# Kernel optimization log

Measured on AMD Instinct MI355X. Metric: run time of the kernel, lower is better.

The kernel has to match this reference:

```python
import jax, jax.numpy as jnp
import numpy as np

WINDOW_SIZE = 11
DATA_RANGE = 1.0
CHANNELS = 3


def _gaussian_window(window_size=WINDOW_SIZE, channel=CHANNELS):
    # 1D gaussian with sigma=1.0, normalized, then outer product -> 2D window
    x = np.arange(window_size)
    g = np.exp(-(x - window_size // 2) ** 2 / (2.0 * 1.0 ** 2))
    g = g / g.sum()
    w2d = np.outer(g, g)  # [K, K]
    # depthwise kernel in OIHW: [C, 1, K, K]
    w = np.broadcast_to(w2d, (channel, 1, window_size, window_size)).copy()
    return jnp.asarray(w, dtype=jnp.float32)


def _depthwise_conv(x, window):
    pad = WINDOW_SIZE // 2
    return jax.lax.conv_general_dilated(
        x, window,
        window_strides=(1, 1),
        padding=[(pad, pad), (pad, pad)],
        feature_group_count=CHANNELS,
        dimension_numbers=("NCHW", "OIHW", "NCHW"),
    )


def setup_inputs() -> dict:
    key = jax.random.key(0)
    k1, k2 = jax.random.split(key)
    pred = jax.random.uniform(k1, (16, 3, 512, 512), dtype=jnp.float32)
    target = jax.random.uniform(k2, (16, 3, 512, 512), dtype=jnp.float32)
    return {"pred": pred, "target": target}


def reference(pred, target):
    window = _gaussian_window()
    mu_x = _depthwise_conv(pred, window)
    mu_y = _depthwise_conv(target, window)
    sigma_x = _depthwise_conv(pred * pred, window) - mu_x * mu_x
    sigma_y = _depthwise_conv(target * target, window) - mu_y * mu_y
    sigma_xy = _depthwise_conv(pred * target, window) - mu_x * mu_y
    C1 = (0.01 * DATA_RANGE) ** 2
    C2 = (0.03 * DATA_RANGE) ** 2
    # NOTE: faithful to source, which (non-standardly) squares the variances in the denominator
    ssim_map = (2 * mu_x * mu_y + C1) * (2 * sigma_xy + C2) / (
        (mu_x * mu_x + mu_y * mu_y + C1) * (sigma_x * sigma_x + sigma_y * sigma_y + C2)
    )
    return ssim_map.mean()
```

## Files before the change

kernel.cpp:

```cpp
#include <hip/hip_runtime.h>
#include <stdint.h>


#define HH 512
#define WW 512
#define PLANES 48
#define TW 64
#define TH 16
#define RR 5
#define KK 11
#define HALO_W 74
#define TRP 28
#define RBW 76
#define NBLOCKS (PLANES * (WW / TW) * (HH / TH))
#define NTHREADS 256
#define NSTAGE (HALO_W * 7)
#define NITEMS1 (HALO_W * 2)
#define TOTAL_ELEMS (PLANES * HH * WW)

typedef _Float16 half2v __attribute__((ext_vector_type(2)));
typedef float float2v __attribute__((ext_vector_type(2)));

constexpr float G_[KK] = {
    1.4867195147342977e-06f, 1.3383022576488537e-04f, 4.4318484119380075e-03f,
    5.3990966513188063e-02f, 2.4197072451914337e-01f, 3.9894228040143270e-01f,
    2.4197072451914337e-01f, 5.3990966513188063e-02f, 4.4318484119380075e-03f,
    1.3383022576488537e-04f, 1.4867195147342977e-06f};

__device__ __forceinline__ half2v u2h(uint32_t u) {
  return __builtin_bit_cast(half2v, u);
}
__device__ __forceinline__ uint32_t packrtn(float a, float b) {
  half2v h = {(_Float16)a, (_Float16)b};
  return __builtin_bit_cast(uint32_t, h);
}

__global__ __launch_bounds__(NTHREADS, 4) void ssim_tile_kernel(
    const float* __restrict__ pred, const float* __restrict__ targ,
    float* __restrict__ partial) {
  __shared__ __align__(16) float spT[HALO_W][TRP];
  __shared__ __align__(16) float stT[HALO_W][TRP];
  __shared__ __align__(16) uint2 rbAB[TH][RBW];
  __shared__ __align__(16) float rbC[TH][RBW];
  __shared__ float wsums[4];

  const int tid = threadIdx.x;
  const int bid = blockIdx.x;
  const int plane = bid >> 8;
  const int tile = bid & 255;
  const int x0 = (tile & 7) * TW;
  const int y0 = (tile >> 3) * TH;
  const float* pp = pred + (size_t)plane * (HH * WW);
  const float* tp = targ + (size_t)plane * (HH * WW);

  const bool interior = (x0 >= 64) && (x0 <= 384) && (y0 >= 16) && (y0 <= 480);

  if (interior) {
    for (int i = tid; i < NSTAGE; i += NTHREADS) {
      const int c = i % HALO_W;
      const int rg = i / HALO_W;
      const float* pb = pp + (y0 - RR + 4 * rg) * WW + (x0 - RR + c);
      const float* tb = tp + (y0 - RR + 4 * rg) * WW + (x0 - RR + c);
      float4 pv, tv;
      pv.x = pb[0]; pv.y = pb[WW]; pv.z = pb[2 * WW]; pv.w = pb[3 * WW];
      tv.x = tb[0]; tv.y = tb[WW]; tv.z = tb[2 * WW]; tv.w = tb[3 * WW];
      *reinterpret_cast<float4*>(&spT[c][4 * rg]) = pv;
      *reinterpret_cast<float4*>(&stT[c][4 * rg]) = tv;
    }
  } else {
    for (int i = tid; i < NSTAGE; i += NTHREADS) {
      const int c = i % HALO_W;
      const int rg = i / HALO_W;
      const int gx = x0 - RR + c;
      const bool xok = (gx >= 0) && (gx < WW);
      float4 pv = make_float4(0.f, 0.f, 0.f, 0.f);
      float4 tv = pv;
      if (xok) {
#pragma unroll
        for (int w = 0; w < 4; ++w) {
          const int gy = y0 - RR + 4 * rg + w;
          if (gy >= 0 && gy < HH) {
            reinterpret_cast<float*>(&pv)[w] = pp[gy * WW + gx];
            reinterpret_cast<float*>(&tv)[w] = tp[gy * WW + gx];
          }
        }
      }
      *reinterpret_cast<float4*>(&spT[c][4 * rg]) = pv;
      *reinterpret_cast<float4*>(&stT[c][4 * rg]) = tv;
    }
  }
  __syncthreads();

  if (tid < NITEMS1) {
    const int c = (tid < HALO_W) ? tid : (tid - HALO_W);
    const int g = (tid < HALO_W) ? 0 : 1;
    const int yb = g * 8;

    float pv[20], tv[20];
#pragma unroll
    for (int h = 0; h < 5; ++h) {
      *reinterpret_cast<float4*>(&pv[4 * h]) =
          *reinterpret_cast<const float4*>(&spT[c][yb + 4 * h]);
      *reinterpret_cast<float4*>(&tv[4 * h]) =
          *reinterpret_cast<const float4*>(&stT[c][yb + 4 * h]);
    }

    float2v s01[8] = {{0,0},{0,0},{0,0},{0,0},{0,0},{0,0},{0,0},{0,0}};
    float2v s23[8] = {{0,0},{0,0},{0,0},{0,0},{0,0},{0,0},{0,0},{0,0}};
    float s4[8] = {0,0,0,0,0,0,0,0};
#pragma unroll
    for (int q = 0; q < 18; ++q) {
      const float a = pv[q];
      const float b = tv[q];
      const float2v av = {a, b};
      const float2v sq = av * av;
      const float ab = a * b;
#pragma unroll
      for (int j = 0; j < 8; ++j) {
        if (q < j || q > j + 10) continue;
        const float w = G_[q - j];
        const float2v w2 = {w, w};
        s01[j] = __builtin_elementwise_fma(w2, av, s01[j]);
        s23[j] = __builtin_elementwise_fma(w2, sq, s23[j]);
        s4[j] = fmaf(w, ab, s4[j]);
      }
    }

#pragma unroll
    for (int j = 0; j < 8; ++j) {
      uint2 u;
      u.x = packrtn(s01[j].x, s01[j].y);
      u.y = packrtn(s23[j].x, s23[j].y);
      rbAB[yb + j][c] = u;
      rbC[yb + j][c] = s4[j];
    }
  }
  __syncthreads();

  float lsum = 0.f;
  {
    const int m = tid & 15;
    const int y = tid >> 4;
    const int cb = m << 2;

    uint2 qv[14];
#pragma unroll
    for (int h = 0; h < 7; ++h) {
      uint4 w = *reinterpret_cast<const uint4*>(&rbAB[y][cb + 2 * h]);
      qv[2*h]   = make_uint2(w.x, w.y);
      qv[2*h+1] = make_uint2(w.z, w.w);
    }
    float cv[16];
#pragma unroll
    for (int h = 0; h < 4; ++h) {
      *reinterpret_cast<float4*>(&cv[4*h]) =
          *reinterpret_cast<const float4*>(&rbC[y][cb + 4 * h]);
    }

    float2v fa[14], fb[14];
#pragma unroll
    for (int k = 0; k < 14; ++k) {
      half2v ha = u2h(qv[k].x), hb = u2h(qv[k].y);
      fa[k] = float2v{(float)ha.x, (float)ha.y};
      fb[k] = float2v{(float)hb.x, (float)hb.y};
    }

    float2v accA[4], accB[4];
    float sC[4];
#pragma unroll
    for (int j = 0; j < 4; ++j) {
      float2v a = {0, 0}, b = {0, 0};
      float c = 0.f;
#pragma unroll
      for (int k = 0; k < KK; ++k) {
        const float2v w2 = {G_[k], G_[k]};
        a = __builtin_elementwise_fma(w2, fa[j + k], a);
        b = __builtin_elementwise_fma(w2, fb[j + k], b);
        c = fmaf(G_[k], cv[j + k], c);
      }
      accA[j] = a; accB[j] = b; sC[j] = c;
    }

    const float C1 = 1.0e-4f;
    const float C2 = 9.0e-4f;
#pragma unroll
    for (int j = 0; j < 4; ++j) {
      const float mu_x = accA[j].x;
      const float mu_y = accA[j].y;
      const float2v sv = __builtin_elementwise_fma(-accA[j], accA[j], accB[j]);
      const float sxy = sC[j] - mu_x * mu_y;
      const float num = (2.f * mu_x * mu_y + C1) * (2.f * sxy + C2);
      const float den = (mu_x * mu_x + mu_y * mu_y + C1) *
                        (fmaf(sv.x, sv.x, fmaf(sv.y, sv.y, C2)));
      lsum = fmaf(num, __builtin_amdgcn_rcpf(den), lsum);
    }
  }

#pragma unroll
  for (int off = 32; off > 0; off >>= 1) lsum += __shfl_xor(lsum, off, 64);
  if ((tid & 63) == 0) wsums[tid >> 6] = lsum;
  __syncthreads();
  if (tid == 0)
    partial[bid] = (wsums[0] + wsums[1]) + (wsums[2] + wsums[3]);
}

__global__ __launch_bounds__(1024) void ssim_reduce_kernel(
    const float* __restrict__ partial, float* __restrict__ out) {
  float s = 0.f;
  for (int i = threadIdx.x; i < NBLOCKS; i += 1024) s += partial[i];
#pragma unroll
  for (int off = 32; off > 0; off >>= 1) s += __shfl_xor(s, off, 64);
  __shared__ float ws[16];
  if ((threadIdx.x & 63) == 0) ws[threadIdx.x >> 6] = s;
  __syncthreads();
  if (threadIdx.x == 0) {
    float t = 0.f;
#pragma unroll
    for (int i = 0; i < 16; ++i) t += ws[i];
    out[0] = t * (1.0f / (float)TOTAL_ELEMS);
  }
}

extern "C" void kernel_launch(void* const* d_in, const int* in_sizes, int n_in,
                              void* d_out, int out_size, void* d_ws,
                              size_t ws_size, hipStream_t stream) {
  const float* pred = (const float*)d_in[0];
  const float* targ = (const float*)d_in[1];
  float* out = (float*)d_out;
  float* partial = (float*)d_ws;

  ssim_tile_kernel<<<NBLOCKS, NTHREADS, 0, stream>>>(pred, targ, partial);
  ssim_reduce_kernel<<<1, 1024, 0, stream>>>(partial, out);
}
```

Measured before the change: 67.19 us.

## Store vertical-pass intermediates in fp32 instead of packed fp16 and restructure staging loop

The intermediate row buffers for mu and second moments are now kept as fp32 float2 arrays instead of packed half precision, which removes the pack and unpack conversions and the fp16 rounding error on the intermediate sums. The staging loop replaces its div/mod indexing with incremental column and row-group stepping. In exchange, shared memory per block grows, which may lower occupancy, and the second pass issues more LDS reads.

```diff
diff --git a/kernel.cpp b/kernel.cpp
--- a/kernel.cpp
+++ b/kernel.cpp
@@ -11,14 +11,13 @@
 #define KK 11
 #define HALO_W 74
 #define TRP 28
-#define RBW 76
+#define RBW 74
+#define RCW 76
 #define NBLOCKS (PLANES * (WW / TW) * (HH / TH))
 #define NTHREADS 256
-#define NSTAGE (HALO_W * 7)
 #define NITEMS1 (HALO_W * 2)
 #define TOTAL_ELEMS (PLANES * HH * WW)
 
-typedef _Float16 half2v __attribute__((ext_vector_type(2)));
 typedef float float2v __attribute__((ext_vector_type(2)));
 
 constexpr float G_[KK] = {
@@ -27,21 +26,14 @@
     2.4197072451914337e-01f, 5.3990966513188063e-02f, 4.4318484119380075e-03f,
     1.3383022576488537e-04f, 1.4867195147342977e-06f};
 
-__device__ __forceinline__ half2v u2h(uint32_t u) {
-  return __builtin_bit_cast(half2v, u);
-}
-__device__ __forceinline__ uint32_t packrtn(float a, float b) {
-  half2v h = {(_Float16)a, (_Float16)b};
-  return __builtin_bit_cast(uint32_t, h);
-}
-
 __global__ __launch_bounds__(NTHREADS, 4) void ssim_tile_kernel(
     const float* __restrict__ pred, const float* __restrict__ targ,
     float* __restrict__ partial) {
   __shared__ __align__(16) float spT[HALO_W][TRP];
   __shared__ __align__(16) float stT[HALO_W][TRP];
-  __shared__ __align__(16) uint2 rbAB[TH][RBW];
-  __shared__ __align__(16) float rbC[TH][RBW];
+  __shared__ __align__(16) float2v rbA2[TH][RBW];
+  __shared__ __align__(16) float2v rbB2[TH][RBW];
+  __shared__ __align__(16) float rbC[TH][RCW];
   __shared__ float wsums[4];
 
   const int tid = threadIdx.x;
@@ -55,38 +47,42 @@
 
   const bool interior = (x0 >= 64) && (x0 <= 384) && (y0 >= 16) && (y0 <= 480);
 
-  if (interior) {
-    for (int i = tid; i < NSTAGE; i += NTHREADS) {
-      const int c = i % HALO_W;
-      const int rg = i / HALO_W;
-      const float* pb = pp + (y0 - RR + 4 * rg) * WW + (x0 - RR + c);
-      const float* tb = tp + (y0 - RR + 4 * rg) * WW + (x0 - RR + c);
-      float4 pv, tv;
-      pv.x = pb[0]; pv.y = pb[WW]; pv.z = pb[2 * WW]; pv.w = pb[3 * WW];
-      tv.x = tb[0]; tv.y = tb[WW]; tv.z = tb[2 * WW]; tv.w = tb[3 * WW];
-      *reinterpret_cast<float4*>(&spT[c][4 * rg]) = pv;
-      *reinterpret_cast<float4*>(&stT[c][4 * rg]) = tv;
-    }
-  } else {
-    for (int i = tid; i < NSTAGE; i += NTHREADS) {
-      const int c = i % HALO_W;
-      const int rg = i / HALO_W;
-      const int gx = x0 - RR + c;
-      const bool xok = (gx >= 0) && (gx < WW);
-      float4 pv = make_float4(0.f, 0.f, 0.f, 0.f);
-      float4 tv = pv;
-      if (xok) {
-#pragma unroll
-        for (int w = 0; w < 4; ++w) {
-          const int gy = y0 - RR + 4 * rg + w;
-          if (gy >= 0 && gy < HH) {
-            reinterpret_cast<float*>(&pv)[w] = pp[gy * WW + gx];
-            reinterpret_cast<float*>(&tv)[w] = tp[gy * WW + gx];
+  {
+    int c = tid % HALO_W;
+    int rg = tid / HALO_W;
+    if (interior) {
+      while (rg < 7) {
+        const float* pb = pp + (y0 - RR + 4 * rg) * WW + (x0 - RR + c);
+        const float* tb = tp + (y0 - RR + 4 * rg) * WW + (x0 - RR + c);
+        float4 pv, tv;
+        pv.x = pb[0]; pv.y = pb[WW]; pv.z = pb[2 * WW]; pv.w = pb[3 * WW];
+        tv.x = tb[0]; tv.y = tb[WW]; tv.z = tb[2 * WW]; tv.w = tb[3 * WW];
+        *reinterpret_cast<float4*>(&spT[c][4 * rg]) = pv;
+        *reinterpret_cast<float4*>(&stT[c][4 * rg]) = tv;
+        c += 34; rg += 3;
+        if (c >= HALO_W) { c -= HALO_W; ++rg; }
+      }
+    } else {
+      while (rg < 7) {
+        const int gx = x0 - RR + c;
+        const bool xok = (gx >= 0) && (gx < WW);
+        float4 pv = make_float4(0.f, 0.f, 0.f, 0.f);
+        float4 tv = pv;
+        if (xok) {
+#pragma unroll
+          for (int w = 0; w < 4; ++w) {
+            const int gy = y0 - RR + 4 * rg + w;
+            if (gy >= 0 && gy < HH) {
+              reinterpret_cast<float*>(&pv)[w] = pp[gy * WW + gx];
+              reinterpret_cast<float*>(&tv)[w] = tp[gy * WW + gx];
+            }
           }
         }
-      }
-      *reinterpret_cast<float4*>(&spT[c][4 * rg]) = pv;
-      *reinterpret_cast<float4*>(&stT[c][4 * rg]) = tv;
+        *reinterpret_cast<float4*>(&spT[c][4 * rg]) = pv;
+        *reinterpret_cast<float4*>(&stT[c][4 * rg]) = tv;
+        c += 34; rg += 3;
+        if (c >= HALO_W) { c -= HALO_W; ++rg; }
+      }
     }
   }
   __syncthreads();
@@ -128,10 +124,8 @@
 
 #pragma unroll
     for (int j = 0; j < 8; ++j) {
-      uint2 u;
-      u.x = packrtn(s01[j].x, s01[j].y);
-      u.y = packrtn(s23[j].x, s23[j].y);
-      rbAB[yb + j][c] = u;
+      rbA2[yb + j][c] = s01[j];
+      rbB2[yb + j][c] = s23[j];
       rbC[yb + j][c] = s4[j];
     }
   }
@@ -143,26 +137,17 @@
     const int y = tid >> 4;
     const int cb = m << 2;
 
-    uint2 qv[14];
-#pragma unroll
-    for (int h = 0; h < 7; ++h) {
-      uint4 w = *reinterpret_cast<const uint4*>(&rbAB[y][cb + 2 * h]);
-      qv[2*h]   = make_uint2(w.x, w.y);
-      qv[2*h+1] = make_uint2(w.z, w.w);
+    float2v fa[14], fb[14];
+#pragma unroll
+    for (int k = 0; k < 14; ++k) {
+      fa[k] = rbA2[y][cb + k];
+      fb[k] = rbB2[y][cb + k];
     }
     float cv[16];
 #pragma unroll
     for (int h = 0; h < 4; ++h) {
-      *reinterpret_cast<float4*>(&cv[4*h]) =
+      *reinterpret_cast<float4*>(&cv[4 * h]) =
           *reinterpret_cast<const float4*>(&rbC[y][cb + 4 * h]);
-    }
-
-    float2v fa[14], fb[14];
-#pragma unroll
-    for (int k = 0; k < 14; ++k) {
-      half2v ha = u2h(qv[k].x), hb = u2h(qv[k].y);
-      fa[k] = float2v{(float)ha.x, (float)ha.y};
-      fb[k] = float2v{(float)hb.x, (float)hb.y};
     }
 
     float2v accA[4], accB[4];
```

Measured after the change: 68.41 us. Within noise of the previous version (+1.8%).
